# Kernel optimization log

Hardware: AMD Instinct MI355X
Metric: run time of the kernel (lower is better)

Reference implementation:

```python
import jax, jax.numpy as jnp
import numpy as np

N = 100000   # nodes
E = 1600000  # edges
D = 64       # input feature dim
H = 64       # hidden dim
C = 10       # classes
G = 1000     # graphs in batch


def setup_inputs() -> dict:
    key = jax.random.key(0)
    ks = jax.random.split(key, 10)
    x = jax.random.normal(ks[0], (N, D), dtype=jnp.float32)
    edge_index = jax.random.randint(ks[1], (2, E), 0, N, dtype=jnp.int32)
    batch = jnp.sort(jax.random.randint(ks[2], (N,), 0, G, dtype=jnp.int32))
    W1 = 0.1 * jax.random.normal(ks[3], (H, D), dtype=jnp.float32)
    W2 = 0.1 * jax.random.normal(ks[4], (H, H), dtype=jnp.float32)
    W3 = 0.1 * jax.random.normal(ks[5], (H, H), dtype=jnp.float32)
    Wf = 0.1 * jax.random.normal(ks[6], (C, H), dtype=jnp.float32)
    b1 = jnp.zeros((H,), jnp.float32)
    b2 = jnp.zeros((H,), jnp.float32)
    b3 = jnp.zeros((H,), jnp.float32)
    bf = jnp.zeros((C,), jnp.float32)
    return {"x": x, "edge_index": edge_index, "batch": batch,
            "W1": W1, "b1": b1, "W2": W2, "b2": b2, "W3": W3, "b3": b3,
            "Wf": Wf, "bf": bf}


def _gcn_layer(h, W, b, src, dst, dinv):
    # GCNConv: xw = h @ W.T; symmetric norm with self-loops; bias after aggregation.
    xw = h @ W.T                                   # [N, H]
    norm = dinv[src] * dinv[dst]                   # [E]
    msg = xw[src] * norm[:, None]                  # [E, H] gather
    agg = jax.ops.segment_sum(msg, dst, num_segments=N)  # scatter-add
    agg = agg + xw * (dinv * dinv)[:, None]        # self-loop contribution
    return agg + b


def reference(x, edge_index, batch, W1, b1, W2, b2, W3, b3, Wf, bf):
    src, dst = edge_index[0], edge_index[1]
    # degree (dst side) including self-loop, as in PyG gcn_norm
    deg = jax.ops.segment_sum(jnp.ones((E,), x.dtype), dst, num_segments=N) + 1.0
    dinv = jax.lax.rsqrt(deg)

    # dropout is identity in eval mode
    h1 = jax.nn.relu(_gcn_layer(x, W1, b1, src, dst, dinv))
    h2 = jax.nn.relu(_gcn_layer(h1, W2, b2, src, dst, dinv))
    h3 = jax.nn.relu(_gcn_layer(h2, W3, b3, src, dst, dinv))

    # global mean pool over graphs
    counts = jax.ops.segment_sum(jnp.ones((N,), x.dtype), batch, num_segments=G)
    pooled = jax.ops.segment_sum(h3, batch, num_segments=G)
    pooled = pooled / jnp.clip(counts, 1.0)[:, None]   # [G, H]

    ffn_output = jax.nn.relu(pooled @ Wf.T + bf)        # [G, C]
    soft = jax.nn.softmax(ffn_output, axis=1)
    return (h1, h2, h3, pooled, ffn_output, soft)
```

## Files before the change

### kernel.cpp

```cpp
#include <hip/hip_runtime.h>
#include <hip/hip_bf16.h>
#include <math.h>

#define NN 100000
#define NE 1600000
#define HD 64
#define NG 1000
#define NC 10

#define NB 782
#define NBLK 196
#define EPB 8164

typedef __attribute__((ext_vector_type(8))) short bf16x8;
typedef __attribute__((ext_vector_type(4))) float f32x4;

__device__ __forceinline__ unsigned short f32_to_bf16(float f) {
    union { float f; unsigned u; } c; c.f = f;
    unsigned u = c.u;
    u += 0x7FFFu + ((u >> 16) & 1u);
    return (unsigned short)(u >> 16);
}
#define BFLO(u) __uint_as_float((u) << 16)
#define BFHI(u) __uint_as_float((u) & 0xFFFF0000u)

__global__ __launch_bounds__(256) void hist_buckets(const int* __restrict__ dst,
                                                    int* __restrict__ hist)
{
    __shared__ int cnt[NB];
    int t = threadIdx.x, blk = blockIdx.x;
    for (int i = t; i < NB; i += 256) cnt[i] = 0;
    __syncthreads();
    int e0 = blk * EPB;
    int e1 = e0 + EPB; if (e1 > NE) e1 = NE;
    for (int e = e0 + t; e < e1; e += 256) atomicAdd(&cnt[dst[e] >> 7], 1);
    __syncthreads();
    for (int i = t; i < NB; i += 256) hist[(size_t)i * NBLK + blk] = cnt[i];
}

__global__ __launch_bounds__(256) void bucket_total(const int* __restrict__ hist,
                                                    int* __restrict__ btotal)
{
    int w = (blockIdx.x * 256 + threadIdx.x) >> 6;
    int lane = threadIdx.x & 63;
    if (w >= NB) return;
    const int* row = hist + (size_t)w * NBLK;
    int s = 0;
    for (int i = lane; i < NBLK; i += 64) s += row[i];
#pragma unroll
    for (int off = 32; off; off >>= 1) s += __shfl_xor(s, off);
    if (lane == 0) btotal[w] = s;
}

__global__ __launch_bounds__(1024) void scan_totals(const int* __restrict__ btotal,
                                                    int* __restrict__ bucketoff)
{
    __shared__ int sm[1024];
    int t = threadIdx.x;
    int v = (t < NB) ? btotal[t] : 0;
    sm[t] = v;
    __syncthreads();
    for (int off = 1; off < 1024; off <<= 1) {
        int u = (t >= off) ? sm[t - off] : 0;
        __syncthreads();
        sm[t] += u;
        __syncthreads();
    }
    if (t <= NB) bucketoff[t] = sm[t] - ((t < NB) ? v : 0);
}

__global__ __launch_bounds__(256) void scan_hist(int* __restrict__ hist,
                                                 const int* __restrict__ bucketoff)
{
    int w = (blockIdx.x * 256 + threadIdx.x) >> 6;
    int lane = threadIdx.x & 63;
    if (w >= NB) return;
    int run = bucketoff[w];
    int* row = hist + (size_t)w * NBLK;
    for (int c0 = 0; c0 < NBLK; c0 += 64) {
        int idx = c0 + lane;
        int v = (idx < NBLK) ? row[idx] : 0;
        int incl = v;
#pragma unroll
        for (int off = 1; off < 64; off <<= 1) {
            int u = __shfl_up(incl, off);
            if (lane >= off) incl += u;
        }
        if (idx < NBLK) row[idx] = run + incl - v;
        run += __shfl(incl, 63);
    }
}

__global__ __launch_bounds__(256) void bin_edges(const int* __restrict__ src,
                                                 const int* __restrict__ dst,
                                                 const int* __restrict__ hist,
                                                 unsigned* __restrict__ pairs)
{
    __shared__ int cur[NB];
    int t = threadIdx.x, blk = blockIdx.x;
    for (int i = t; i < NB; i += 256) cur[i] = hist[(size_t)i * NBLK + blk];
    __syncthreads();
    int e0 = blk * EPB;
    int e1 = e0 + EPB; if (e1 > NE) e1 = NE;
    for (int e = e0 + t; e < e1; e += 256) {
        int d = dst[e], s = src[e];
        int b = d >> 7;
        int pos = atomicAdd(&cur[b], 1);
        pairs[pos] = ((unsigned)(d & 127) << 17) | (unsigned)s;
    }
}

__global__ __launch_bounds__(256) void sort_bucket(const int* __restrict__ bucketoff,
                                                   const unsigned* __restrict__ pairs,
                                                   int* __restrict__ rowstart,
                                                   int* __restrict__ srcidx,
                                                   float* __restrict__ dinv)
{
    __shared__ int cnt[1024], boff[1024], wsum[256];
    int b = blockIdx.x, t = threadIdx.x;
    int e0 = bucketoff[b], e1 = bucketoff[b + 1];
    for (int i = t; i < 1024; i += 256) cnt[i] = 0;
    __syncthreads();
    for (int e = e0 + t; e < e1; e += 256) {
        unsigned pk = pairs[e];
        int key = (int)((pk >> 17) << 3) | (int)((pk & 0x1FFFFu) >> 14);
        atomicAdd(&cnt[key], 1);
    }
    __syncthreads();
    int base4 = t * 4;
    int s0 = cnt[base4], s1 = cnt[base4 + 1], s2 = cnt[base4 + 2], s3 = cnt[base4 + 3];
    wsum[t] = s0 + s1 + s2 + s3;
    __syncthreads();
    for (int o = 1; o < 256; o <<= 1) {
        int u = (t >= o) ? wsum[t - o] : 0;
        __syncthreads();
        wsum[t] += u;
        __syncthreads();
    }
    int run = e0 + ((t > 0) ? wsum[t - 1] : 0);
    boff[base4]     = run;
    boff[base4 + 1] = run + s0;
    boff[base4 + 2] = run + s0 + s1;
    boff[base4 + 3] = run + s0 + s1 + s2;
    __syncthreads();
    if (t < 128) {
        int rs = boff[t * 8];
        int re = (t < 127) ? boff[t * 8 + 8] : e1;
        int node = (b << 7) + t;
        if (node < NN) {
            rowstart[node] = rs;
            dinv[node] = rsqrtf((float)(re - rs) + 1.0f);
        }
    }
    if (b == NB - 1 && t == 0) rowstart[NN] = e1;
    __syncthreads();
    for (int e = e0 + t; e < e1; e += 256) {
        unsigned pk = pairs[e];
        int key = (int)((pk >> 17) << 3) | (int)((pk & 0x1FFFFu) >> 14);
        int pos = atomicAdd(&boff[key], 1);
        srcidx[pos] = (int)(pk & 0x1FFFF);
    }
}

__global__ __launch_bounds__(256) void graph_bounds(const int* __restrict__ batch,
                                                    int* __restrict__ gstart)
{
    int i = blockIdx.x * 256 + threadIdx.x;
    if (i >= NN) return;
    int b = batch[i];
    if (i == 0) {
        for (int g = 0; g <= b; ++g) gstart[g] = 0;
    } else {
        int p = batch[i - 1];
        for (int g = p + 1; g <= b; ++g) gstart[g] = i;
    }
    if (i == NN - 1) {
        for (int g = b + 1; g <= NG; ++g) gstart[g] = NN;
    }
}

__global__ __launch_bounds__(256) void gemm_mfma(const float* __restrict__ h,
                                                 const float* __restrict__ W,
                                                 const float* __restrict__ dinv,
                                                 unsigned short* __restrict__ y,
                                                 int nrows)
{
    const int t = threadIdx.x;
    const int lane = t & 63;
    const int wave = t >> 6;
    const int rbase = blockIdx.x * 64;
    const int l15 = lane & 15;
    const int kq  = lane >> 4;

    bf16x8 Bf[4][2];
#pragma unroll
    for (int c = 0; c < 4; ++c) {
#pragma unroll
        for (int kb = 0; kb < 2; ++kb) {
            const float* wp = W + (c * 16 + l15) * 64 + kb * 32 + kq * 8;
            float f[8];
            *(float4*)(f)     = *(const float4*)(wp);
            *(float4*)(f + 4) = *(const float4*)(wp + 4);
            bf16x8 v;
#pragma unroll
            for (int i = 0; i < 8; ++i) v[i] = (short)f32_to_bf16(f[i]);
            Bf[c][kb] = v;
        }
    }

    int arow = rbase + wave * 16 + l15;
    if (arow >= nrows) arow = nrows - 1;
    bf16x8 Af[2];
#pragma unroll
    for (int kb = 0; kb < 2; ++kb) {
        const float* hp = h + (size_t)arow * 64 + kb * 32 + kq * 8;
        float f[8];
        *(float4*)(f)     = *(const float4*)(hp);
        *(float4*)(f + 4) = *(const float4*)(hp + 4);
        bf16x8 v;
#pragma unroll
        for (int i = 0; i < 8; ++i) v[i] = (short)f32_to_bf16(f[i]);
        Af[kb] = v;
    }

    f32x4 acc[4] = {{0.f,0.f,0.f,0.f},{0.f,0.f,0.f,0.f},{0.f,0.f,0.f,0.f},{0.f,0.f,0.f,0.f}};
#pragma unroll
    for (int c = 0; c < 4; ++c) {
        acc[c] = __builtin_amdgcn_mfma_f32_16x16x32_bf16(Af[0], Bf[c][0], acc[c], 0, 0, 0);
        acc[c] = __builtin_amdgcn_mfma_f32_16x16x32_bf16(Af[1], Bf[c][1], acc[c], 0, 0, 0);
    }

    const int drow0 = rbase + wave * 16 + kq * 4;
#pragma unroll
    for (int r = 0; r < 4; ++r) {
        int rg = drow0 + r;
        if (rg < nrows) {
            float d = dinv[rg];
#pragma unroll
            for (int c = 0; c < 4; ++c)
                y[(size_t)rg * 64 + c * 16 + l15] = f32_to_bf16(acc[c][r] * d);
        }
    }
}

__global__ __launch_bounds__(256) void pull_aggr(const int* __restrict__ rowstart,
                                                 const int* __restrict__ srcidx,
                                                 const unsigned* __restrict__ y,
                                                 const float* __restrict__ dinv,
                                                 const float* __restrict__ bias,
                                                 float* __restrict__ hout)
{
    int wid = (blockIdx.x * blockDim.x + threadIdx.x) >> 6;
    int lane = threadIdx.x & 63;
    if (wid >= NN) return;
    const int fl = lane & 31;
    const int half = lane >> 5;

    unsigned su = y[(size_t)wid * 32 + fl];
    float acc0 = half ? 0.f : BFLO(su);
    float acc1 = half ? 0.f : BFHI(su);

    int s0 = rowstart[wid], s1 = rowstart[wid + 1];
    for (int base = s0; base < s1; base += 64) {
        int nb = s1 - base; if (nb > 64) nb = 64;
        int idx = (lane < nb) ? srcidx[base + lane] : 0;
        int j = 0;
        for (; j + 16 <= nb; j += 16) {
            int a0 = __shfl(idx, j + 0),  b0 = __shfl(idx, j + 1);
            int a1 = __shfl(idx, j + 2),  b1 = __shfl(idx, j + 3);
            int a2 = __shfl(idx, j + 4),  b2 = __shfl(idx, j + 5);
            int a3 = __shfl(idx, j + 6),  b3 = __shfl(idx, j + 7);
            int a4 = __shfl(idx, j + 8),  b4 = __shfl(idx, j + 9);
            int a5 = __shfl(idx, j + 10), b5 = __shfl(idx, j + 11);
            int a6 = __shfl(idx, j + 12), b6 = __shfl(idx, j + 13);
            int a7 = __shfl(idx, j + 14), b7 = __shfl(idx, j + 15);
            int e0 = half ? b0 : a0, e1 = half ? b1 : a1;
            int e2 = half ? b2 : a2, e3 = half ? b3 : a3;
            int e4 = half ? b4 : a4, e5 = half ? b5 : a5;
            int e6 = half ? b6 : a6, e7 = half ? b7 : a7;
            unsigned u0 = y[(size_t)e0 * 32 + fl];
            unsigned u1 = y[(size_t)e1 * 32 + fl];
            unsigned u2 = y[(size_t)e2 * 32 + fl];
            unsigned u3 = y[(size_t)e3 * 32 + fl];
            unsigned u4 = y[(size_t)e4 * 32 + fl];
            unsigned u5 = y[(size_t)e5 * 32 + fl];
            unsigned u6 = y[(size_t)e6 * 32 + fl];
            unsigned u7 = y[(size_t)e7 * 32 + fl];
            acc0 += BFLO(u0); acc1 += BFHI(u0);
            acc0 += BFLO(u1); acc1 += BFHI(u1);
            acc0 += BFLO(u2); acc1 += BFHI(u2);
            acc0 += BFLO(u3); acc1 += BFHI(u3);
            acc0 += BFLO(u4); acc1 += BFHI(u4);
            acc0 += BFLO(u5); acc1 += BFHI(u5);
            acc0 += BFLO(u6); acc1 += BFHI(u6);
            acc0 += BFLO(u7); acc1 += BFHI(u7);
        }
        for (; j + 2 <= nb; j += 2) {
            int a = __shfl(idx, j), b = __shfl(idx, j + 1);
            int e = half ? b : a;
            unsigned u = y[(size_t)e * 32 + fl];
            acc0 += BFLO(u); acc1 += BFHI(u);
        }
        if (j < nb) {
            int a = __shfl(idx, j);
            unsigned u = y[(size_t)a * 32 + fl];
            if (!half) { acc0 += BFLO(u); acc1 += BFHI(u); }
        }
    }

    acc0 += __shfl_xor(acc0, 32);
    acc1 += __shfl_xor(acc1, 32);
    if (half == 0) {
        float d = dinv[wid];
        float2 bb = ((const float2*)bias)[fl];
        float2 v;
        v.x = fmaxf(fmaf(acc0, d, bb.x), 0.f);
        v.y = fmaxf(fmaf(acc1, d, bb.y), 0.f);
        ((float2*)hout)[(size_t)wid * 32 + fl] = v;
    }
}

__global__ __launch_bounds__(256) void pool_ffn(const float* __restrict__ h3,
                                                const int* __restrict__ gstart,
                                                const float* __restrict__ Wf,
                                                const float* __restrict__ bf,
                                                float* __restrict__ pooled,
                                                float* __restrict__ ffn,
                                                float* __restrict__ soft)
{
    __shared__ float part[4][64];
    int g = blockIdx.x;
    int t = threadIdx.x, wv = t >> 6, lane = t & 63;
    int start = gstart[g], end = gstart[g + 1];

    float acc = 0.f;
    for (int n = start + wv; n < end; n += 4) acc += h3[(size_t)n * 64 + lane];
    part[wv][lane] = acc;
    __syncthreads();
    if (wv != 0) return;

    float a = part[0][lane] + part[1][lane] + part[2][lane] + part[3][lane];
    float cnt = (float)(end - start);
    float pv = a / fmaxf(cnt, 1.0f);
    pooled[g * 64 + lane] = pv;

    float f = 0.f;
#pragma unroll
    for (int cls = 0; cls < NC; ++cls) {
        float v = pv * Wf[cls * 64 + lane];
#pragma unroll
        for (int off = 32; off; off >>= 1) v += __shfl_xor(v, off);
        if (lane == cls) f = v;
    }
    float fb = (lane < NC) ? fmaxf(f + bf[lane], 0.f) : -INFINITY;
    if (lane < NC) ffn[g * NC + lane] = fb;

    float m = fb;
#pragma unroll
    for (int off = 32; off; off >>= 1) m = fmaxf(m, __shfl_xor(m, off));
    float e = (lane < NC) ? expf(fb - m) : 0.f;
    float s = e;
#pragma unroll
    for (int off = 32; off; off >>= 1) s += __shfl_xor(s, off);
    if (lane < NC) soft[g * NC + lane] = e / s;
}

extern "C" void kernel_launch(void* const* d_in, const int* in_sizes, int n_in,
                              void* d_out, int out_size, void* d_ws, size_t ws_size,
                              hipStream_t stream) {
    const float* x   = (const float*)d_in[0];
    const int*   ei  = (const int*)d_in[1];
    const int*   bat = (const int*)d_in[2];
    const float* W1  = (const float*)d_in[3];
    const float* b1  = (const float*)d_in[4];
    const float* W2  = (const float*)d_in[5];
    const float* b2  = (const float*)d_in[6];
    const float* W3  = (const float*)d_in[7];
    const float* b3  = (const float*)d_in[8];
    const float* Wf  = (const float*)d_in[9];
    const float* bf  = (const float*)d_in[10];

    const int* src = ei;
    const int* dst = ei + NE;

    float* out    = (float*)d_out;
    float* h1     = out;
    float* h2     = out + (size_t)NN * HD;
    float* h3     = out + (size_t)2 * NN * HD;
    float* pooled = out + (size_t)3 * NN * HD;
    float* ffn    = pooled + (size_t)NG * HD;
    float* soft   = ffn + (size_t)NG * NC;

    char* ws = (char*)d_ws;
    float*          dinv      = (float*)(ws + 0);
    int*            rowstart  = (int*)(ws + 400000);
    int*            srcidx    = (int*)(ws + 800016);
    unsigned short* y         = (unsigned short*)(ws + 7200016);
    int*            gstart    = (int*)(ws + 20000016);
    unsigned*       pairs     = (unsigned*)(ws + 7200016);
    int*            hist      = (int*)(ws + 13600016);
    int*            btotal    = (int*)(ws + 14213104);
    int*            bucketoff = (int*)(ws + 14216232);

    hist_buckets<<<NBLK, 256, 0, stream>>>(dst, hist);
    bucket_total<<<(NB + 3) / 4, 256, 0, stream>>>(hist, btotal);
    scan_totals<<<1, 1024, 0, stream>>>(btotal, bucketoff);
    scan_hist<<<(NB + 3) / 4, 256, 0, stream>>>(hist, bucketoff);
    bin_edges<<<NBLK, 256, 0, stream>>>(src, dst, hist, pairs);
    sort_bucket<<<NB, 256, 0, stream>>>(bucketoff, pairs, rowstart, srcidx, dinv);
    graph_bounds<<<(NN + 255) / 256, 256, 0, stream>>>(bat, gstart);

    const int gemmGrid = (NN + 63) / 64;
    const int aggrGrid = (NN + 3) / 4;

    gemm_mfma<<<gemmGrid, 256, 0, stream>>>(x, W1, dinv, y, NN);
    pull_aggr<<<aggrGrid, 256, 0, stream>>>(rowstart, srcidx, (const unsigned*)y, dinv, b1, h1);

    gemm_mfma<<<gemmGrid, 256, 0, stream>>>(h1, W2, dinv, y, NN);
    pull_aggr<<<aggrGrid, 256, 0, stream>>>(rowstart, srcidx, (const unsigned*)y, dinv, b2, h2);

    gemm_mfma<<<gemmGrid, 256, 0, stream>>>(h2, W3, dinv, y, NN);
    pull_aggr<<<aggrGrid, 256, 0, stream>>>(rowstart, srcidx, (const unsigned*)y, dinv, b3, h3);

    pool_ffn<<<NG, 256, 0, stream>>>(h3, gstart, Wf, bf, pooled, ffn, soft);
}
```

Baseline: 296.0 us.

## Map half-waves to nodes in aggregation and simplify bucket sort keys

The pull aggregation now gives each 32-lane half-wave its own node, and each half-wave processes two nodes in sequence. This removes the cross-half reduction and the shuffle-select logic, and cuts idle lanes for low-degree nodes. The bucket sort counts by destination only (128 keys) rather than a 1024-key sub-sort on source bits, which shortens the scan and lowers LDS use. The cost is that srcidx is no longer ordered by source within each row, so gather locality may suffer, and there is less memory parallelism per node.

After: 286.2 us, median of 2. 3.3% less time.

```diff
diff --git a/kernel.cpp b/kernel.cpp
--- a/kernel.cpp
+++ b/kernel.cpp
@@ -116,48 +116,35 @@
                                                    int* __restrict__ srcidx,
                                                    float* __restrict__ dinv)
 {
-    __shared__ int cnt[1024], boff[1024], wsum[256];
+    __shared__ int cnt[128], off[128], cur[128];
     int b = blockIdx.x, t = threadIdx.x;
     int e0 = bucketoff[b], e1 = bucketoff[b + 1];
-    for (int i = t; i < 1024; i += 256) cnt[i] = 0;
+    if (t < 128) cnt[t] = 0;
+    __syncthreads();
+    for (int e = e0 + t; e < e1; e += 256) atomicAdd(&cnt[pairs[e] >> 17], 1);
+    __syncthreads();
+    if (t < 128) off[t] = cnt[t];
+    __syncthreads();
+    for (int o = 1; o < 128; o <<= 1) {
+        int u = (t < 128 && t >= o) ? off[t - o] : 0;
+        __syncthreads();
+        if (t < 128) off[t] += u;
+        __syncthreads();
+    }
+    if (t < 128) {
+        int ex = e0 + off[t] - cnt[t];
+        cur[t] = ex;
+        int node = (b << 7) + t;
+        if (node < NN) {
+            rowstart[node] = ex;
+            dinv[node] = rsqrtf((float)cnt[t] + 1.0f);
+        }
+    }
+    if (b == NB - 1 && t == 0) rowstart[NN] = e1;
     __syncthreads();
     for (int e = e0 + t; e < e1; e += 256) {
         unsigned pk = pairs[e];
-        int key = (int)((pk >> 17) << 3) | (int)((pk & 0x1FFFFu) >> 14);
-        atomicAdd(&cnt[key], 1);
-    }
-    __syncthreads();
-    int base4 = t * 4;
-    int s0 = cnt[base4], s1 = cnt[base4 + 1], s2 = cnt[base4 + 2], s3 = cnt[base4 + 3];
-    wsum[t] = s0 + s1 + s2 + s3;
-    __syncthreads();
-    for (int o = 1; o < 256; o <<= 1) {
-        int u = (t >= o) ? wsum[t - o] : 0;
-        __syncthreads();
-        wsum[t] += u;
-        __syncthreads();
-    }
-    int run = e0 + ((t > 0) ? wsum[t - 1] : 0);
-    boff[base4]     = run;
-    boff[base4 + 1] = run + s0;
-    boff[base4 + 2] = run + s0 + s1;
-    boff[base4 + 3] = run + s0 + s1 + s2;
-    __syncthreads();
-    if (t < 128) {
-        int rs = boff[t * 8];
-        int re = (t < 127) ? boff[t * 8 + 8] : e1;
-        int node = (b << 7) + t;
-        if (node < NN) {
-            rowstart[node] = rs;
-            dinv[node] = rsqrtf((float)(re - rs) + 1.0f);
-        }
-    }
-    if (b == NB - 1 && t == 0) rowstart[NN] = e1;
-    __syncthreads();
-    for (int e = e0 + t; e < e1; e += 256) {
-        unsigned pk = pairs[e];
-        int key = (int)((pk >> 17) << 3) | (int)((pk & 0x1FFFFu) >> 14);
-        int pos = atomicAdd(&boff[key], 1);
+        int pos = atomicAdd(&cur[pk >> 17], 1);
         srcidx[pos] = (int)(pk & 0x1FFFF);
     }
 }
@@ -243,6 +230,7 @@
     }
 }
 
+#define NPN 2
 __global__ __launch_bounds__(256) void pull_aggr(const int* __restrict__ rowstart,
                                                  const int* __restrict__ srcidx,
                                                  const unsigned* __restrict__ y,
@@ -250,73 +238,55 @@
                                                  const float* __restrict__ bias,
                                                  float* __restrict__ hout)
 {
-    int wid = (blockIdx.x * blockDim.x + threadIdx.x) >> 6;
-    int lane = threadIdx.x & 63;
-    if (wid >= NN) return;
-    const int fl = lane & 31;
-    const int half = lane >> 5;
-
-    unsigned su = y[(size_t)wid * 32 + fl];
-    float acc0 = half ? 0.f : BFLO(su);
-    float acc1 = half ? 0.f : BFHI(su);
-
-    int s0 = rowstart[wid], s1 = rowstart[wid + 1];
-    for (int base = s0; base < s1; base += 64) {
-        int nb = s1 - base; if (nb > 64) nb = 64;
-        int idx = (lane < nb) ? srcidx[base + lane] : 0;
-        int j = 0;
-        for (; j + 16 <= nb; j += 16) {
-            int a0 = __shfl(idx, j + 0),  b0 = __shfl(idx, j + 1);
-            int a1 = __shfl(idx, j + 2),  b1 = __shfl(idx, j + 3);
-            int a2 = __shfl(idx, j + 4),  b2 = __shfl(idx, j + 5);
-            int a3 = __shfl(idx, j + 6),  b3 = __shfl(idx, j + 7);
-            int a4 = __shfl(idx, j + 8),  b4 = __shfl(idx, j + 9);
-            int a5 = __shfl(idx, j + 10), b5 = __shfl(idx, j + 11);
-            int a6 = __shfl(idx, j + 12), b6 = __shfl(idx, j + 13);
-            int a7 = __shfl(idx, j + 14), b7 = __shfl(idx, j + 15);
-            int e0 = half ? b0 : a0, e1 = half ? b1 : a1;
-            int e2 = half ? b2 : a2, e3 = half ? b3 : a3;
-            int e4 = half ? b4 : a4, e5 = half ? b5 : a5;
-            int e6 = half ? b6 : a6, e7 = half ? b7 : a7;
-            unsigned u0 = y[(size_t)e0 * 32 + fl];
-            unsigned u1 = y[(size_t)e1 * 32 + fl];
-            unsigned u2 = y[(size_t)e2 * 32 + fl];
-            unsigned u3 = y[(size_t)e3 * 32 + fl];
-            unsigned u4 = y[(size_t)e4 * 32 + fl];
-            unsigned u5 = y[(size_t)e5 * 32 + fl];
-            unsigned u6 = y[(size_t)e6 * 32 + fl];
-            unsigned u7 = y[(size_t)e7 * 32 + fl];
-            acc0 += BFLO(u0); acc1 += BFHI(u0);
-            acc0 += BFLO(u1); acc1 += BFHI(u1);
-            acc0 += BFLO(u2); acc1 += BFHI(u2);
-            acc0 += BFLO(u3); acc1 += BFHI(u3);
-            acc0 += BFLO(u4); acc1 += BFHI(u4);
-            acc0 += BFLO(u5); acc1 += BFHI(u5);
-            acc0 += BFLO(u6); acc1 += BFHI(u6);
-            acc0 += BFLO(u7); acc1 += BFHI(u7);
-        }
-        for (; j + 2 <= nb; j += 2) {
-            int a = __shfl(idx, j), b = __shfl(idx, j + 1);
-            int e = half ? b : a;
-            unsigned u = y[(size_t)e * 32 + fl];
-            acc0 += BFLO(u); acc1 += BFHI(u);
-        }
-        if (j < nb) {
-            int a = __shfl(idx, j);
-            unsigned u = y[(size_t)a * 32 + fl];
-            if (!half) { acc0 += BFLO(u); acc1 += BFHI(u); }
-        }
-    }
-
-    acc0 += __shfl_xor(acc0, 32);
-    acc1 += __shfl_xor(acc1, 32);
-    if (half == 0) {
-        float d = dinv[wid];
-        float2 bb = ((const float2*)bias)[fl];
+    int hw = (blockIdx.x * blockDim.x + threadIdx.x) >> 5;
+    int fl = threadIdx.x & 31;
+    int hb = threadIdx.x & 32;
+    float2 bb = ((const float2*)bias)[fl];
+
+#pragma unroll 1
+    for (int i = 0; i < NPN; ++i) {
+        int n = hw * NPN + i;
+        if (n >= NN) return;
+        int s0 = rowstart[n], s1 = rowstart[n + 1];
+        unsigned su = y[(size_t)n * 32 + fl];
+        float acc0 = BFLO(su), acc1 = BFHI(su);
+        for (int base = s0; base < s1; base += 32) {
+            int nb = s1 - base; if (nb > 32) nb = 32;
+            int idx = (fl < nb) ? srcidx[base + fl] : 0;
+            int j = 0;
+            for (; j + 8 <= nb; j += 8) {
+                int e0 = __shfl(idx, hb + j + 0), e1 = __shfl(idx, hb + j + 1);
+                int e2 = __shfl(idx, hb + j + 2), e3 = __shfl(idx, hb + j + 3);
+                int e4 = __shfl(idx, hb + j + 4), e5 = __shfl(idx, hb + j + 5);
+                int e6 = __shfl(idx, hb + j + 6), e7 = __shfl(idx, hb + j + 7);
+                unsigned u0 = y[(size_t)e0 * 32 + fl];
+                unsigned u1 = y[(size_t)e1 * 32 + fl];
+                unsigned u2 = y[(size_t)e2 * 32 + fl];
+                unsigned u3 = y[(size_t)e3 * 32 + fl];
+                unsigned u4 = y[(size_t)e4 * 32 + fl];
+                unsigned u5 = y[(size_t)e5 * 32 + fl];
+                unsigned u6 = y[(size_t)e6 * 32 + fl];
+                unsigned u7 = y[(size_t)e7 * 32 + fl];
+                acc0 += BFLO(u0); acc1 += BFHI(u0);
+                acc0 += BFLO(u1); acc1 += BFHI(u1);
+                acc0 += BFLO(u2); acc1 += BFHI(u2);
+                acc0 += BFLO(u3); acc1 += BFHI(u3);
+                acc0 += BFLO(u4); acc1 += BFHI(u4);
+                acc0 += BFLO(u5); acc1 += BFHI(u5);
+                acc0 += BFLO(u6); acc1 += BFHI(u6);
+                acc0 += BFLO(u7); acc1 += BFHI(u7);
+            }
+            for (; j < nb; ++j) {
+                int e = __shfl(idx, hb + j);
+                unsigned u = y[(size_t)e * 32 + fl];
+                acc0 += BFLO(u); acc1 += BFHI(u);
+            }
+        }
+        float d = dinv[n];
         float2 v;
         v.x = fmaxf(fmaf(acc0, d, bb.x), 0.f);
         v.y = fmaxf(fmaf(acc1, d, bb.y), 0.f);
-        ((float2*)hout)[(size_t)wid * 32 + fl] = v;
+        ((float2*)hout)[(size_t)n * 32 + fl] = v;
     }
 }
 
@@ -411,7 +381,7 @@
     graph_bounds<<<(NN + 255) / 256, 256, 0, stream>>>(bat, gstart);
 
     const int gemmGrid = (NN + 63) / 64;
-    const int aggrGrid = (NN + 3) / 4;
+    const int aggrGrid = (NN + 8 * NPN - 1) / (8 * NPN);
 
     gemm_mfma<<<gemmGrid, 256, 0, stream>>>(x, W1, dinv, y, NN);
     pull_aggr<<<aggrGrid, 256, 0, stream>>>(rowstart, srcidx, (const unsigned*)y, dinv, b1, h1);
```
